# Kernel tuning notes

Measured on AMD Instinct MI355X. Metric: run time of the kernel, lower is better.

## Reference

```python
import jax, jax.numpy as jnp
import numpy as np

B, S, HID = 2, 4096, 2048
H, D = 16, 128
BS = 64            # block_size
SR = 0.5           # sparsity_ratio
NB = S // BS       # number of diagonal blocks
SCALE = D ** -0.5


def setup_inputs() -> dict:
    key = jax.random.key(0)
    ks = jax.random.split(key, 7)
    s = 0.02
    return {
        "hidden_states": jax.random.normal(ks[0], (B, S, HID), jnp.float32),
        "Wq": jax.random.normal(ks[1], (HID, H * D), jnp.float32) * s,
        "Wk": jax.random.normal(ks[2], (HID, H * D), jnp.float32) * s,
        "Wv": jax.random.normal(ks[3], (HID, H * D), jnp.float32) * s,
        "Wo": jax.random.normal(ks[4], (H * D, HID), jnp.float32) * s,
        "Wr": jax.random.normal(ks[5], (HID, H), jnp.float32) * s,   # block_router weight
        "br": jax.random.normal(ks[6], (H,), jnp.float32) * s,       # block_router bias
    }


def reference(hidden_states, Wq, Wk, Wv, Wo, Wr, br):
    # projections: torch Linear(x) == x @ W^T; weights stored pre-transposed here
    q = (hidden_states @ Wq).reshape(B, S, H, D).transpose(0, 2, 1, 3)  # [B,H,S,D]
    k = (hidden_states @ Wk).reshape(B, S, H, D).transpose(0, 2, 1, 3)
    v = (hidden_states @ Wv).reshape(B, S, H, D).transpose(0, 2, 1, 3)

    # per-head routing score, mean-pooled over batch (as in torch: routing_scores[:, h].mean())
    routing = jax.nn.sigmoid(hidden_states.mean(axis=1) @ Wr + br)      # [B,H]
    head_score = routing.mean(axis=0)                                   # [H]
    eff_sparsity = SR * (1.0 - head_score * 0.5)
    # torch: max(1, int(block_size * eff)); positive -> floor == int truncation
    attend_count = jnp.maximum(1, jnp.floor(BS * eff_sparsity).astype(jnp.int32))  # [H]

    # block-diagonal attention: only within-block scores are ever finite, so we
    # never materialize the full SxS matrix (softmax over -inf elsewhere is a no-op)
    qb = q.reshape(B, H, NB, BS, D)
    kb = k.reshape(B, H, NB, BS, D)
    vb = v.reshape(B, H, NB, BS, D)
    scores = jnp.einsum("bhnqd,bhnkd->bhnqk", qb, kb) * SCALE           # [B,H,NB,BS,BS]

    # rank of each key within its row (descending); keep == variable-k top-k mask.
    order = jnp.argsort(-scores, axis=-1)
    rank = jnp.argsort(order, axis=-1)
    keep = rank < attend_count[None, :, None, None, None]
    # non-top-k in-block entries are scattered as 0.0 (not -inf) in the original
    masked = jnp.where(keep, scores, 0.0)

    probs = jax.nn.softmax(masked.astype(jnp.float32), axis=-1).astype(q.dtype)
    out_b = jnp.einsum("bhnqk,bhnkd->bhnqd", probs, vb)                 # [B,H,NB,BS,D]
    out = out_b.reshape(B, H, S, D).transpose(0, 2, 1, 3).reshape(B, S, H * D)
    return out @ Wo
```

## Files before the change

### kernel.cpp

```cpp
#include <hip/hip_runtime.h>
#include <hip/hip_bf16.h>
#include <cstdint>
#include <cstddef>

#define B_   2
#define S_   4096
#define HIDN 2048
#define H_   16
#define D_   128
#define NB_  64
#define MTOT 8192
#define QKVN 6144
#define SCALE_ 0.08838834764831845f

typedef unsigned short ushort_t;
typedef __attribute__((ext_vector_type(8))) short short8;
typedef __attribute__((ext_vector_type(8))) ushort_t ushort8;
typedef __attribute__((ext_vector_type(4))) float f32x4;

__device__ inline float b2f(ushort_t x){ union{unsigned u; float f;} v; v.u=((unsigned)x)<<16; return v.f; }
__device__ inline ushort_t f2b(float f){ union{unsigned u; float f;} v; v.f=f; unsigned r=(v.u + 0x7FFF + ((v.u>>16)&1))>>16; return (ushort_t)r; }

#define MFMA_BF16(a,b,c) __builtin_amdgcn_mfma_f32_16x16x32_bf16((a),(b),(c),0,0,0)

__device__ inline void async16(const ushort_t* g, ushort_t* l){
  __builtin_amdgcn_global_load_lds(
      (const __attribute__((address_space(1))) void*)g,
      (__attribute__((address_space(3))) void*)l, 16, 0, 0);
}

__global__ void bsa_convpart(const float* __restrict__ hs, ushort_t* __restrict__ hsB,
                             float* __restrict__ part){
  int t = threadIdx.x;
  int c  = blockIdx.x*512 + t*2;
  int sc = blockIdx.y;
  int b  = blockIdx.z;
  const float* p = hs  + ((size_t)b*S_ + (size_t)sc*128)*HIDN + c;
  ushort_t*    q = hsB + ((size_t)b*S_ + (size_t)sc*128)*HIDN + c;
  float s0=0.f, s1=0.f;
  #pragma unroll 8
  for (int i=0;i<128;i++){
    float2 v = *(const float2*)(p + (size_t)i*HIDN);
    s0 += v.x; s1 += v.y;
    unsigned pk = (unsigned)f2b(v.x) | ((unsigned)f2b(v.y)<<16);
    *(unsigned*)(q + (size_t)i*HIDN) = pk;
  }
  part[((b*32+sc)*HIDN)+c]   = s0;
  part[((b*32+sc)*HIDN)+c+1] = s1;
}

__global__ void bsa_router(const float* __restrict__ part, const float* __restrict__ Wr,
                           const float* __restrict__ br, int* __restrict__ counts){
  __shared__ float cm[2*HIDN];
  __shared__ float sig[2*H_];
  int t = threadIdx.x;
  for (int i=t; i<2*HIDN; i+=256){
    int b = i>>11, c = i&(HIDN-1);
    float s=0.f;
    for (int j=0;j<32;j++) s += part[((b*32+j)*HIDN)+c];
    cm[b*HIDN+c] = s * (1.0f/S_);
  }
  __syncthreads();
  {
    int g = t>>3;
    int sl = t&7;
    int b = g>>4, h = g&15;
    float acc = 0.f;
    for (int c=sl; c<HIDN; c+=8) acc += cm[b*HIDN+c]*Wr[c*H_+h];
    acc += __shfl_xor(acc, 4);
    acc += __shfl_xor(acc, 2);
    acc += __shfl_xor(acc, 1);
    if (sl==0) sig[g] = 1.f/(1.f+expf(-(acc + br[h])));
  }
  __syncthreads();
  if (t < H_){
    float score = 0.5f*(sig[t] + sig[H_+t]);
    float eff = 0.5f*(1.0f - score*0.5f);
    int ac = (int)floorf(64.f*eff);
    if (ac < 1) ac = 1;
    counts[t] = ac;
  }
}

__global__ void bsa_transpose(const float* w0, const float* w1, const float* w2, const float* w3,
                              ushort_t* o0, ushort_t* o1, ushort_t* o2, ushort_t* o3){
  const float* src; ushort_t* dst;
  switch(blockIdx.z){
    case 0: src=w0; dst=o0; break;
    case 1: src=w1; dst=o1; break;
    case 2: src=w2; dst=o2; break;
    default: src=w3; dst=o3; break;
  }
  __shared__ ushort_t tile[64*72];
  int t = threadIdx.x;
  int r0 = blockIdx.y*64, c0 = blockIdx.x*64;
  for (int it=0; it<16; it++){
    int f = it*256 + t;
    int r = f>>6, c = f&63;
    tile[r*72+c] = f2b(src[(size_t)(r0+r)*HIDN + (c0+c)]);
  }
  __syncthreads();
  for (int it=0; it<16; it++){
    int f = it*256 + t;
    int cc = f>>6, rr = f&63;
    dst[(size_t)(c0+cc)*HIDN + (r0+rr)] = tile[rr*72+cc];
  }
}


#define SBAR asm volatile("s_barrier" ::: "memory")
#define WVM4 asm volatile("s_waitcnt vmcnt(4)" ::: "memory")
#define WVM0 asm volatile("s_waitcnt vmcnt(0)" ::: "memory")
#define PHI  __builtin_amdgcn_s_setprio(1)
#define PLO  __builtin_amdgcn_s_setprio(0)

__device__ __forceinline__ short8 lds_frag(const ushort_t* buf, int row, int kb){
  int off = ((row<<7) + kb) ^ ((row&7)<<4);
  return *(const short8*)((const char*)buf + off);
}

__device__ __forceinline__ void rd_a(short8 (&a)[4][2], const ushort_t* buf, int r0, int l16, int quad){
  #pragma unroll
  for (int mi=0; mi<4; mi++)
    #pragma unroll
    for (int ks=0; ks<2; ks++)
      a[mi][ks] = lds_frag(buf, r0 + mi*16 + l16, ks*64 + quad*16);
}
__device__ __forceinline__ void rd_b(short8 (&b)[2][2], const ushort_t* buf, int r0, int l16, int quad){
  #pragma unroll
  for (int ni=0; ni<2; ni++)
    #pragma unroll
    for (int ks=0; ks<2; ks++)
      b[ni][ks] = lds_frag(buf, r0 + ni*16 + l16, ks*64 + quad*16);
}
__device__ __forceinline__ void mm8(f32x4 (&acc)[8][4], const short8 (&a)[4][2],
                                    const short8 (&b)[2][2], int mo, int no){
  #pragma unroll
  for (int mi=0; mi<4; mi++)
    #pragma unroll
    for (int ni=0; ni<2; ni++){
      acc[mo+mi][no+ni] = MFMA_BF16(a[mi][0], b[ni][0], acc[mo+mi][no+ni]);
      acc[mo+mi][no+ni] = MFMA_BF16(a[mi][1], b[ni][1], acc[mo+mi][no+ni]);
    }
}
__device__ __forceinline__ void stage_half(ushort_t* ldsHalf, const ushort_t* g,
                                           int K, int w, int roff, int coff){
  async16(g + (size_t)(w*16 + roff)*K + coff,     ldsHalf + (w*2+0)*512);
  async16(g + (size_t)(w*16 + 8 + roff)*K + coff, ldsHalf + (w*2+1)*512);
}

template<int F32OUT>
__global__ __launch_bounds__(512, 2) void bsa_gemm8(const ushort_t* __restrict__ A,
                                                    const ushort_t* __restrict__ BT,
                                                    void* __restrict__ Cv,
                                                    int M, int N, int K){
  extern __shared__ __align__(16) ushort_t sm[];
  ushort_t* A0  = sm;
  ushort_t* A1  = sm + 16384;
  ushort_t* Bb0 = sm + 32768;
  ushort_t* Bb1 = sm + 49152;

  int t = threadIdx.x;
  int w = t>>6, lane = t&63, quad = lane>>4, l16 = lane&15;
  int wr = w>>2, wc = w&3;

  int nbx = N>>8;
  int nwg = (M>>8)*nbx;
  int bid = blockIdx.x;
  int swz = (bid&7)*(nwg>>3) + (bid>>3);
  int bx = swz % nbx, by = swz / nbx;
  int m0 = by<<8, n0 = bx<<8;

  const ushort_t* Ag = A  + (size_t)m0*K;
  const ushort_t* Bg = BT + (size_t)n0*K;
  int roff = lane>>3;
  int coff = ((lane&7) ^ roff) << 3;

  f32x4 acc[8][4] = {};
  short8 a[4][2], b0[2][2], b1[2][2];

  stage_half(A0,        Ag,                      K, w, roff, coff);
  stage_half(A0+8192,   Ag + (size_t)128*K,      K, w, roff, coff);
  stage_half(Bb0,       Bg,                      K, w, roff, coff);
  stage_half(Bb0+8192,  Bg + (size_t)128*K,      K, w, roff, coff);
  stage_half(Bb1,       Bg + 64,                 K, w, roff, coff);
  stage_half(Bb1+8192,  Bg + (size_t)128*K + 64, K, w, roff, coff);
  WVM4;
  SBAR;

  int nit = K>>7;
  #pragma unroll 1
  for (int i=0; i<nit; i++){
    bool notlast = (i+1 < nit);
    int kA  = (2*i+1)*64;
    int kN0 = (2*i+2)*64;
    int kN1 = (2*i+3)*64;
    rd_a(a, A0, wr*128, l16, quad);
    rd_b(b0, Bb0, wc*64, l16, quad);
    stage_half(A1, Ag + kA, K, w, roff, coff);
    PHI; mm8(acc, a, b0, 0,0); PLO;
    SBAR;
    rd_b(b1, Bb0, wc*64+32, l16, quad);
    stage_half(A1+8192, Ag + (size_t)128*K + kA, K, w, roff, coff);
    PHI; mm8(acc, a, b1, 0,2); PLO;
    SBAR;
    rd_a(a, A0, wr*128+64, l16, quad);
    if (notlast) stage_half(Bb0, Bg + kN0, K, w, roff, coff);
    PHI; mm8(acc, a, b0, 4,0); PLO;
    SBAR;
    if (notlast) stage_half(Bb0+8192, Bg + (size_t)128*K + kN0, K, w, roff, coff);
    PHI; mm8(acc, a, b1, 4,2); PLO;
    if (notlast) { WVM4; } else { WVM0; }
    SBAR;
    rd_a(a, A1, wr*128, l16, quad);
    rd_b(b0, Bb1, wc*64, l16, quad);
    if (notlast) stage_half(A0, Ag + kN0, K, w, roff, coff);
    PHI; mm8(acc, a, b0, 0,0); PLO;
    SBAR;
    rd_b(b1, Bb1, wc*64+32, l16, quad);
    if (notlast) stage_half(A0+8192, Ag + (size_t)128*K + kN0, K, w, roff, coff);
    PHI; mm8(acc, a, b1, 0,2); PLO;
    SBAR;
    rd_a(a, A1, wr*128+64, l16, quad);
    if (notlast) stage_half(Bb1, Bg + kN1, K, w, roff, coff);
    PHI; mm8(acc, a, b0, 4,0); PLO;
    SBAR;
    if (notlast) stage_half(Bb1+8192, Bg + (size_t)128*K + kN1, K, w, roff, coff);
    PHI; mm8(acc, a, b1, 4,2); PLO;
    if (notlast) { WVM4; } else { WVM0; }
    SBAR;
  }

  #pragma unroll
  for (int mi=0; mi<8; mi++)
    #pragma unroll
    for (int ni=0; ni<4; ni++){
      int m = m0 + wr*128 + mi*16 + quad*4;
      int n = n0 + wc*64 + ni*16 + l16;
      #pragma unroll
      for (int r=0;r<4;r++){
        if (F32OUT) ((float*)Cv)[(size_t)(m+r)*N + n] = acc[mi][ni][r];
        else        ((ushort_t*)Cv)[(size_t)(m+r)*N + n] = f2b(acc[mi][ni][r]);
      }
    }
}

__global__ __launch_bounds__(256) void bsa_attn(const ushort_t* __restrict__ QKV,
                                                const int* __restrict__ counts,
                                                ushort_t* __restrict__ O){
  __shared__ __align__(16) ushort_t regA[64*136];
  __shared__ __align__(16) ushort_t regB[64*136];
  __shared__ __align__(16) ushort_t Ps[64*72];
  float* Sc = (float*)regA;

  int t = threadIdx.x, w = t>>6, lane = t&63, quad = lane>>4, l16 = lane&15;
  int bid = blockIdx.x;
  int b  = bid>>10;
  int h  = (bid>>6)&15;
  int nb = bid&63;
  size_t qbase = ((size_t)b*S_ + (size_t)nb*64)*QKVN + (size_t)h*D_;
  size_t obase = ((size_t)b*S_ + (size_t)nb*64)*HIDN + (size_t)h*D_;

  int4 vre[4];
  #pragma unroll
  for (int it=0; it<4; it++){
    int f = it*256 + t;
    int r = f>>4, c = (f&15)*8;
    vre[it] = *(const int4*)(QKV + qbase + 4096 + (size_t)r*QKVN + c);
  }

  #pragma unroll
  for (int it=0; it<4; it++){
    int f = it*256 + t;
    int r = f>>4, c = (f&15)*8;
    *(int4*)(&regA[r*136+c]) = *(const int4*)(QKV + qbase +        (size_t)r*QKVN + c);
    *(int4*)(&regB[r*136+c]) = *(const int4*)(QKV + qbase + 2048 + (size_t)r*QKVN + c);
  }
  __syncthreads();

  f32x4 sacc[4] = {};
  #pragma unroll
  for (int ks=0; ks<4; ks++){
    short8 afr = *(const short8*)(&regA[(w*16 + l16)*136 + ks*32 + quad*8]);
    #pragma unroll
    for (int nt=0; nt<4; nt++){
      short8 bfr = *(const short8*)(&regB[(nt*16 + l16)*136 + ks*32 + quad*8]);
      sacc[nt] = MFMA_BF16(afr, bfr, sacc[nt]);
    }
  }
  __syncthreads();

  #pragma unroll
  for (int nt=0; nt<4; nt++)
    #pragma unroll
    for (int r=0;r<4;r++)
      Sc[(w*16 + quad*4 + r)*68 + nt*16 + l16] = sacc[nt][r]*SCALE_;
  #pragma unroll
  for (int it=0; it<4; it++){
    int f = it*256 + t;
    int r = f>>4, c = (f&15)*8;
    *(int4*)(&regB[r*136+c]) = vre[it];
  }

  int cnt = counts[h];
  for (int g=0; g<4; g++){
    float s[4], v[4];
    #pragma unroll
    for (int rr=0; rr<4; rr++){
      s[rr] = Sc[(w*16 + g*4 + rr)*68 + lane];
      v[rr] = s[rr];
    }
    #pragma unroll
    for (int k=2; k<=64; k<<=1){
      #pragma unroll
      for (int m=k>>1; m>=1; m>>=1){
        #pragma unroll
        for (int rr=0; rr<4; rr++){
          float o = __shfl_xor(v[rr], m);
          bool keepMin = (((lane & k)==0) == ((lane & m)==0));
          float lo = fminf(v[rr], o), hi = fmaxf(v[rr], o);
          v[rr] = keepMin ? lo : hi;
        }
      }
    }
    #pragma unroll
    for (int rr=0; rr<4; rr++){
      float T = __shfl(v[rr], 64 - cnt);
      unsigned long long gt = __ballot(s[rr] > T);
      unsigned long long eq = __ballot(s[rr] == T);
      int G = __popcll(gt);
      int eqr = __popcll(eq & ((1ull<<lane)-1ull));
      bool keep = (s[rr] > T) || ((s[rr] == T) && (eqr < cnt - G));
      float m = keep ? s[rr] : 0.0f;
      float mx = fmaxf(__shfl(v[rr], 63), 0.0f);
      float e = __expf(m - mx);
      float sum = e;
      #pragma unroll
      for (int off=32; off; off>>=1) sum += __shfl_xor(sum, off);
      Ps[(w*16 + g*4 + rr)*72 + lane] = f2b(e/sum);
    }
  }
  __syncthreads();

  f32x4 oacc[4][2] = {};
  #pragma unroll
  for (int ks=0; ks<2; ks++){
    short8 bv[2];
    #pragma unroll
    for (int jj=0; jj<2; jj++){
      int n = (w*2+jj)*16 + l16;
      short8 x;
      #pragma unroll
      for (int j=0;j<8;j++){
        int k = ks*32 + quad*8 + j;
        x[j] = (short)regB[k*136 + n];
      }
      bv[jj] = x;
    }
    #pragma unroll
    for (int mt=0; mt<4; mt++){
      short8 aP = *(const short8*)(&Ps[(mt*16 + l16)*72 + ks*32 + quad*8]);
      #pragma unroll
      for (int jj=0; jj<2; jj++)
        oacc[mt][jj] = MFMA_BF16(aP, bv[jj], oacc[mt][jj]);
    }
  }
  #pragma unroll
  for (int mt=0; mt<4; mt++)
    #pragma unroll
    for (int jj=0; jj<2; jj++){
      int row = mt*16 + quad*4;
      int col = (w*2+jj)*16 + l16;
      #pragma unroll
      for (int r=0;r<4;r++)
        O[obase + (size_t)(row+r)*HIDN + col] = f2b(oacc[mt][jj][r]);
    }
}

extern "C" void kernel_launch(void* const* d_in, const int* in_sizes, int n_in,
                              void* d_out, int out_size, void* d_ws, size_t ws_size,
                              hipStream_t stream) {
  const float* hs = (const float*)d_in[0];
  const float* Wq = (const float*)d_in[1];
  const float* Wk = (const float*)d_in[2];
  const float* Wv = (const float*)d_in[3];
  const float* Wo = (const float*)d_in[4];
  const float* Wr = (const float*)d_in[5];
  const float* br = (const float*)d_in[6];
  float* out = (float*)d_out;
  char* ws = (char*)d_ws;

  const size_t MB = 1024u*1024u;
  float*    part   = (float*)(ws + 0);
  int*      counts = (int*)(ws + 512u*1024u);
  ushort_t* hsB    = (ushort_t*)(ws + 1*MB);
  ushort_t* WqT    = (ushort_t*)(ws + 33*MB);
  ushort_t* WkT    = (ushort_t*)(ws + 41*MB);
  ushort_t* WvT    = (ushort_t*)(ws + 49*MB);
  ushort_t* WoT    = (ushort_t*)(ws + 57*MB);
  ushort_t* QKV    = (ushort_t*)(ws + 65*MB);
  ushort_t* AO     = hsB;

  static bool attr_done = false;
  if (!attr_done){
    hipFuncSetAttribute((const void*)&bsa_gemm8<0>,
                        hipFuncAttributeMaxDynamicSharedMemorySize, 131072);
    hipFuncSetAttribute((const void*)&bsa_gemm8<1>,
                        hipFuncAttributeMaxDynamicSharedMemorySize, 131072);
    attr_done = true;
  }

  bsa_convpart  <<<dim3(4,32,2),  256, 0, stream>>>(hs, hsB, part);
  bsa_router    <<<1,             256, 0, stream>>>(part, Wr, br, counts);
  bsa_transpose <<<dim3(32,32,4), 256, 0, stream>>>(Wq,Wk,Wv,Wo, WqT,WkT,WvT,WoT);
  bsa_gemm8<0><<<dim3(768), 512, 131072, stream>>>(hsB, WqT, (void*)QKV, MTOT, QKVN, 2048);
  bsa_attn      <<<2048,          256, 0, stream>>>(QKV, counts, AO);
  bsa_gemm8<1><<<dim3(256), 512, 131072, stream>>>(AO, WoT, (void*)out, MTOT, 2048, 2048);
}
```

Baseline: 648.6 us.

## Software-pipeline GEMM LDS reads, vectorize router reduction and weight transpose

The GEMM main loop is restructured so that LDS fragment reads for the next sub-step are issued during the current MFMA block, with split half-tile reads interleaved between MFMAs and adjusted vmcnt waits. This is meant to hide LDS latency behind matrix math. Separately, the router uses 1024 threads with float4 loads to reduce the partial sums, and the weight transpose uses a swizzled LDS tile with 16-byte vector stores. The new GEMM barrier and wait placement risks races if a buffer is overwritten before every wave has finished reading it.

```diff
diff --git a/kernel.cpp b/kernel.cpp
--- a/kernel.cpp
+++ b/kernel.cpp
@@ -54,14 +54,21 @@
   __shared__ float cm[2*HIDN];
   __shared__ float sig[2*H_];
   int t = threadIdx.x;
-  for (int i=t; i<2*HIDN; i+=256){
-    int b = i>>11, c = i&(HIDN-1);
-    float s=0.f;
-    for (int j=0;j<32;j++) s += part[((b*32+j)*HIDN)+c];
-    cm[b*HIDN+c] = s * (1.0f/S_);
-  }
-  __syncthreads();
   {
+    int b  = t>>9;
+    int c4 = (t&511)*4;
+    float sx=0.f, sy=0.f, sz=0.f, sw=0.f;
+    for (int j=0;j<32;j++){
+      float4 v = *(const float4*)&part[((b*32+j)*HIDN)+c4];
+      sx+=v.x; sy+=v.y; sz+=v.z; sw+=v.w;
+    }
+    cm[b*HIDN+c4+0]=sx*(1.0f/S_);
+    cm[b*HIDN+c4+1]=sy*(1.0f/S_);
+    cm[b*HIDN+c4+2]=sz*(1.0f/S_);
+    cm[b*HIDN+c4+3]=sw*(1.0f/S_);
+  }
+  __syncthreads();
+  if (t < 256){
     int g = t>>3;
     int sl = t&7;
     int b = g>>4, h = g&15;
@@ -91,25 +98,29 @@
     case 2: src=w2; dst=o2; break;
     default: src=w3; dst=o3; break;
   }
-  __shared__ ushort_t tile[64*72];
+  __shared__ ushort_t tt[64*72];
   int t = threadIdx.x;
   int r0 = blockIdx.y*64, c0 = blockIdx.x*64;
+  #pragma unroll
   for (int it=0; it<16; it++){
     int f = it*256 + t;
     int r = f>>6, c = f&63;
-    tile[r*72+c] = f2b(src[(size_t)(r0+r)*HIDN + (c0+c)]);
-  }
-  __syncthreads();
-  for (int it=0; it<16; it++){
+    tt[c*72 + (r ^ ((c&7)<<3))] = f2b(src[(size_t)(r0+r)*HIDN + (c0+c)]);
+  }
+  __syncthreads();
+  #pragma unroll
+  for (int it=0; it<2; it++){
     int f = it*256 + t;
-    int cc = f>>6, rr = f&63;
-    dst[(size_t)(c0+cc)*HIDN + (r0+rr)] = tile[rr*72+cc];
+    int cc = f>>3, rb = (f&7)<<3;
+    ushort8 v = *(const ushort8*)&tt[cc*72 + (rb ^ ((cc&7)<<3))];
+    *(ushort8*)&dst[(size_t)(c0+cc)*HIDN + r0 + rb] = v;
   }
 }
 
 
 #define SBAR asm volatile("s_barrier" ::: "memory")
 #define WVM4 asm volatile("s_waitcnt vmcnt(4)" ::: "memory")
+#define WVM2 asm volatile("s_waitcnt vmcnt(2)" ::: "memory")
 #define WVM0 asm volatile("s_waitcnt vmcnt(0)" ::: "memory")
 #define PHI  __builtin_amdgcn_s_setprio(1)
 #define PLO  __builtin_amdgcn_s_setprio(0)
@@ -126,6 +137,13 @@
     for (int ks=0; ks<2; ks++)
       a[mi][ks] = lds_frag(buf, r0 + mi*16 + l16, ks*64 + quad*16);
 }
+__device__ __forceinline__ void rd_a2(short8 (&a)[4][2], const ushort_t* buf, int r0, int l16, int quad, int mi0){
+  #pragma unroll
+  for (int mi=mi0; mi<mi0+2; mi++)
+    #pragma unroll
+    for (int ks=0; ks<2; ks++)
+      a[mi][ks] = lds_frag(buf, r0 + mi*16 + l16, ks*64 + quad*16);
+}
 __device__ __forceinline__ void rd_b(short8 (&b)[2][2], const ushort_t* buf, int r0, int l16, int quad){
   #pragma unroll
   for (int ni=0; ni<2; ni++)
@@ -137,6 +155,16 @@
                                     const short8 (&b)[2][2], int mo, int no){
   #pragma unroll
   for (int mi=0; mi<4; mi++)
+    #pragma unroll
+    for (int ni=0; ni<2; ni++){
+      acc[mo+mi][no+ni] = MFMA_BF16(a[mi][0], b[ni][0], acc[mo+mi][no+ni]);
+      acc[mo+mi][no+ni] = MFMA_BF16(a[mi][1], b[ni][1], acc[mo+mi][no+ni]);
+    }
+}
+__device__ __forceinline__ void mm8h(f32x4 (&acc)[8][4], const short8 (&a)[4][2],
+                                     const short8 (&b)[2][2], int mo, int no, int mi0){
+  #pragma unroll
+  for (int mi=mi0; mi<mi0+2; mi++)
     #pragma unroll
     for (int ni=0; ni<2; ni++){
       acc[mo+mi][no+ni] = MFMA_BF16(a[mi][0], b[ni][0], acc[mo+mi][no+ni]);
@@ -187,47 +215,62 @@
   stage_half(Bb1+8192,  Bg + (size_t)128*K + 64, K, w, roff, coff);
   WVM4;
   SBAR;
+  rd_a(a,  A0,  wr*128,    l16, quad);
+  rd_b(b0, Bb0, wc*64,     l16, quad);
+  rd_b(b1, Bb0, wc*64+32,  l16, quad);
 
   int nit = K>>7;
   #pragma unroll 1
   for (int i=0; i<nit; i++){
-    bool notlast = (i+1 < nit);
-    int kA  = (2*i+1)*64;
-    int kN0 = (2*i+2)*64;
-    int kN1 = (2*i+3)*64;
-    rd_a(a, A0, wr*128, l16, quad);
-    rd_b(b0, Bb0, wc*64, l16, quad);
+    bool nl = (i+1 < nit);
+    int kA  = (2*i+1)<<6;
+    int kN0 = (2*i+2)<<6;
+    int kN1 = (2*i+3)<<6;
     stage_half(A1, Ag + kA, K, w, roff, coff);
     PHI; mm8(acc, a, b0, 0,0); PLO;
     SBAR;
-    rd_b(b1, Bb0, wc*64+32, l16, quad);
     stage_half(A1+8192, Ag + (size_t)128*K + kA, K, w, roff, coff);
-    PHI; mm8(acc, a, b1, 0,2); PLO;
-    SBAR;
-    rd_a(a, A0, wr*128+64, l16, quad);
-    if (notlast) stage_half(Bb0, Bg + kN0, K, w, roff, coff);
+    PHI;
+    mm8h(acc, a, b1, 0,2, 0);
+    rd_a2(a, A0, wr*128+64, l16, quad, 0);
+    mm8h(acc, a, b1, 0,2, 2);
+    rd_a2(a, A0, wr*128+64, l16, quad, 2);
+    PLO;
+    WVM4;
+    SBAR;
+    if (nl) stage_half(Bb0, Bg + kN0, K, w, roff, coff);
+    PHI; mm8(acc, a, b1, 4,2); PLO;
+    rd_b(b1, Bb1, wc*64+32, l16, quad);
+    SBAR;
+    if (nl) stage_half(Bb0+8192, Bg + (size_t)128*K + kN0, K, w, roff, coff);
     PHI; mm8(acc, a, b0, 4,0); PLO;
-    SBAR;
-    if (notlast) stage_half(Bb0+8192, Bg + (size_t)128*K + kN0, K, w, roff, coff);
+    rd_b(b0, Bb1, wc*64, l16, quad);
+    if (nl) { WVM4; } else { WVM0; }
+    SBAR;
+    rd_a(a, A1, wr*128, l16, quad);
+    if (nl) stage_half(A0, Ag + kN0, K, w, roff, coff);
+    PHI; mm8(acc, a, b0, 0,0); PLO;
+    SBAR;
+    if (nl) stage_half(A0+8192, Ag + (size_t)128*K + kN0, K, w, roff, coff);
+    PHI;
+    mm8h(acc, a, b1, 0,2, 0);
+    rd_a2(a, A1, wr*128+64, l16, quad, 0);
+    mm8h(acc, a, b1, 0,2, 2);
+    rd_a2(a, A1, wr*128+64, l16, quad, 2);
+    PLO;
+    if (nl) { WVM4; }
+    SBAR;
+    if (nl) stage_half(Bb1, Bg + kN1, K, w, roff, coff);
     PHI; mm8(acc, a, b1, 4,2); PLO;
-    if (notlast) { WVM4; } else { WVM0; }
-    SBAR;
-    rd_a(a, A1, wr*128, l16, quad);
-    rd_b(b0, Bb1, wc*64, l16, quad);
-    if (notlast) stage_half(A0, Ag + kN0, K, w, roff, coff);
-    PHI; mm8(acc, a, b0, 0,0); PLO;
-    SBAR;
-    rd_b(b1, Bb1, wc*64+32, l16, quad);
-    if (notlast) stage_half(A0+8192, Ag + (size_t)128*K + kN0, K, w, roff, coff);
-    PHI; mm8(acc, a, b1, 0,2); PLO;
-    SBAR;
-    rd_a(a, A1, wr*128+64, l16, quad);
-    if (notlast) stage_half(Bb1, Bg + kN1, K, w, roff, coff);
+    if (nl) rd_b(b1, Bb0, wc*64+32, l16, quad);
+    if (nl) { WVM2; }
+    SBAR;
+    if (nl) stage_half(Bb1+8192, Bg + (size_t)128*K + kN1, K, w, roff, coff);
     PHI; mm8(acc, a, b0, 4,0); PLO;
-    SBAR;
-    if (notlast) stage_half(Bb1+8192, Bg + (size_t)128*K + kN1, K, w, roff, coff);
-    PHI; mm8(acc, a, b1, 4,2); PLO;
-    if (notlast) { WVM4; } else { WVM0; }
+    if (nl){
+      rd_b(b0, Bb0, wc*64,  l16, quad);
+      rd_a(a,  A0,  wr*128, l16, quad);
+    }
     SBAR;
   }
 
@@ -411,7 +454,7 @@
   }
 
   bsa_convpart  <<<dim3(4,32,2),  256, 0, stream>>>(hs, hsB, part);
-  bsa_router    <<<1,             256, 0, stream>>>(part, Wr, br, counts);
+  bsa_router    <<<1,            1024, 0, stream>>>(part, Wr, br, counts);
   bsa_transpose <<<dim3(32,32,4), 256, 0, stream>>>(Wq,Wk,Wv,Wo, WqT,WkT,WvT,WoT);
   bsa_gemm8<0><<<dim3(768), 512, 131072, stream>>>(hsB, WqT, (void*)QKV, MTOT, QKVN, 2048);
   bsa_attn      <<<2048,          256, 0, stream>>>(QKV, counts, AO);
```

Measured after the change: 670.6 us. 1.03x slower.
